# Performance work log

Hardware: AMD Instinct MI355X
Metric: run time of the kernel (lower is better)

Reference implementation:

```python
import jax, jax.numpy as jnp
import numpy as np
from jax import lax

B, TENC, TMEL = 32, 512, 400
E, H, A, P, M, F, K = 512, 512, 512, 256, 128, 32, 31


def setup_inputs() -> dict:
    key = jax.random.key(0)
    ks = jax.random.split(key, 20)
    def rn(i, shape, fan_in):
        return jax.random.normal(ks[i], shape, jnp.float32) / np.float32(np.sqrt(fan_in))
    return dict(
        enc_outputs=jax.random.normal(ks[0], (B, TENC, 2 * E), jnp.float32),
        mel_spec_true=jax.random.normal(ks[1], (B, TMEL, M), jnp.float32),
        text_lens=jax.random.randint(ks[2], (B,), 0, TENC),
        mel_spec_lens=jax.random.randint(ks[3], (B,), 0, TMEL),
        max_text_len=TENC,
        pre_w1=rn(4, (M, P), M), pre_w2=rn(5, (P, P), P),
        attn_wi=rn(6, (P + E, 3 * H), P + E), attn_wh=rn(7, (H, 3 * H), H),
        attn_bi=jnp.zeros((3 * H,), jnp.float32), attn_bh=jnp.zeros((3 * H,), jnp.float32),
        q_w=rn(8, (H, A), H), k_w=rn(9, (2 * E, A), 2 * E),
        score_w=rn(10, (A, 1), A), score_b=jnp.zeros((1,), jnp.float32),
        loc_conv_w=rn(11, (F, 2, K), 2 * K), loc_w=rn(12, (F, A), F), loc_b=jnp.zeros((A,), jnp.float32),
        out_wi=rn(13, (A + H, 3 * H), A + H), out_wh=rn(14, (H, 3 * H), H),
        out_bi=jnp.zeros((3 * H,), jnp.float32), out_bh=jnp.zeros((3 * H,), jnp.float32),
        dec_w=rn(15, (H + A, M), H + A), dec_b=jnp.zeros((M,), jnp.float32),
        gate_w=rn(16, (H + A, 1), H + A), gate_b=jnp.zeros((1,), jnp.float32),
    )


def _gru_step(x, h, wi, wh, bi, bh):
    # single-step torch nn.GRU cell; gate order r, z, n
    gi = x @ wi + bi
    gh = h @ wh + bh
    ir, iz, inn = jnp.split(gi, 3, axis=-1)
    hr, hz, hn = jnp.split(gh, 3, axis=-1)
    r = jax.nn.sigmoid(ir + hr)
    z = jax.nn.sigmoid(iz + hz)
    n = jnp.tanh(inn + r * hn)
    return (1.0 - z) * n + z * h


def reference(enc_outputs, mel_spec_true, text_lens, mel_spec_lens, max_text_len,
              pre_w1, pre_w2, attn_wi, attn_wh, attn_bi, attn_bh,
              q_w, k_w, score_w, score_b, loc_conv_w, loc_w, loc_b,
              out_wi, out_wh, out_bi, out_bh, dec_w, dec_b, gate_w, gate_b):
    Bsz, Tenc, _ = enc_outputs.shape
    Tmel = mel_spec_true.shape[1]
    Hd = attn_wh.shape[0]
    Ad = k_w.shape[1]
    pad = (loc_conv_w.shape[2] - 1) // 2

    keys_p = enc_outputs @ k_w                                # [B,Tenc,A]
    enc_mask = jnp.arange(Tenc)[None, :] > text_lens[:, None]  # True = masked (t > len)

    def prenet(x):  # dropout disabled for determinism
        return jax.nn.relu(jax.nn.relu(x @ pre_w1) @ pre_w2)

    dec_in0 = prenet(jnp.zeros((Bsz, mel_spec_true.shape[2]), enc_outputs.dtype))
    carry0 = (jnp.zeros((Bsz, Hd), jnp.float32), jnp.zeros((Bsz, Hd), jnp.float32),
              jnp.zeros((Bsz, Tenc), jnp.float32), jnp.zeros((Bsz, Tenc), jnp.float32),
              jnp.zeros((Bsz, Ad), jnp.float32), dec_in0)

    def step(carry, _):
        h_attn, h_out, att_w, att_cum, ctx, dec_in = carry
        h_attn = _gru_step(jnp.concatenate([dec_in, ctx], -1), h_attn, attn_wi, attn_wh, attn_bi, attn_bh)
        loc_in = jnp.stack([att_w, att_cum], axis=1)           # [B,2,Tenc]
        loc = lax.conv_general_dilated(loc_in, loc_conv_w, (1,), [(pad, pad)],
                                       dimension_numbers=('NCH', 'OIH', 'NCH'))  # [B,F,Tenc]
        loc = jnp.swapaxes(loc, 1, 2) @ loc_w + loc_b          # [B,Tenc,A]
        q = (h_attn @ q_w)[:, None, :]                         # [B,1,A]
        s = (jnp.tanh(q + keys_p + loc) @ score_w + score_b)[..., 0]  # [B,Tenc]
        s = jnp.where(enc_mask, -jnp.inf, s)
        att_w = jax.nn.softmax(s, axis=1)
        ctx = jnp.einsum('bt,bta->ba', att_w, keys_p)
        att_cum = att_cum + att_w
        h_out = _gru_step(jnp.concatenate([h_attn, ctx], -1), h_out, out_wi, out_wh, out_bi, out_bh)
        att_h = jnp.concatenate([h_out, ctx], -1)
        mel = att_h @ dec_w + dec_b                            # [B,M]
        stop = (att_h @ gate_w + gate_b)[:, 0]                 # [B]
        dec_in = prenet(mel)                                   # teacher_force_ratio = 0
        return (h_attn, h_out, att_w, att_cum, ctx, dec_in), (mel, stop, att_w)

    _, (mels, gates, attns) = lax.scan(step, carry0, None, length=Tmel)
    mels = jnp.swapaxes(mels, 0, 1)    # [B,Tmel,M]
    gates = jnp.swapaxes(gates, 0, 1)  # [B,Tmel]
    attns = jnp.swapaxes(attns, 0, 1)  # [B,Tmel,Tenc]
    mel_mask = jnp.arange(Tmel)[None, :] > mel_spec_lens[:, None]
    masked_mel = jnp.where(mel_mask[:, :, None], 0.0, mels)
    masked_gate = jnp.where(mel_mask, 1000.0, gates)
    return masked_mel, masked_gate, attns, mel_mask
```

## Files before the change

kernel.cpp:

```cpp
#include <hip/hip_runtime.h>
#include <hip/hip_fp16.h>
#include <math.h>

#define NBLK 256
#define NTHR 1024

__device__ __forceinline__ float fast_rcp(float x) {
#if __has_builtin(__builtin_amdgcn_rcpf)
  return __builtin_amdgcn_rcpf(x);
#else
  return 1.f / x;
#endif
}
__device__ __forceinline__ float fast_sigmoid(float x) { return fast_rcp(1.f + __expf(-x)); }
__device__ __forceinline__ float fast_tanh(float x) { return 1.f - 2.f * fast_rcp(1.f + __expf(2.f * x)); }

union HU2 { unsigned int u; __half2 h; };
union HU4 { uint4 u; __half2 h[4]; };
__device__ __forceinline__ float2 cvt2(unsigned int u) { HU2 t; t.u = u; return __half22float2(t.h); }

__device__ __forceinline__ void sta(float* p, float v) {
  __hip_atomic_store(p, v, __ATOMIC_RELAXED, __HIP_MEMORY_SCOPE_AGENT);
}
__device__ __forceinline__ float lda(const float* p) {
  return __hip_atomic_load(p, __ATOMIC_RELAXED, __HIP_MEMORY_SCOPE_AGENT);
}
__device__ __forceinline__ int ldai(const int* p) {
  return __hip_atomic_load(p, __ATOMIC_RELAXED, __HIP_MEMORY_SCOPE_AGENT);
}
__device__ __forceinline__ void ntst(float* p, float v) { __builtin_nontemporal_store(v, p); }

struct Params {
  const float *enc, *pre_w1, *pre_w2, *attn_bi, *attn_bh;
  const float *q_w, *k_w, *score_w, *score_b, *conv_w, *loc_w, *loc_b;
  const float *out_bi, *out_bh, *dec_b, *gate_b;
  const float *attn_wi, *attn_wh, *out_wi, *out_wh, *dec_w, *gate_w;
  const int *text_lens, *mel_lens;
  __half *hkeys, *gw1T, *gw2T, *decT, *pre1T, *pre2T, *gateh, *locwh, *qwT;
  float *hA, *hO, *attw, *attcum, *decin, *ebuf, *zpart, *ctxacc, *ctxacc2, *stateZ;
  float *qbuf;
  int *done, *zdone, *done2, *hAdone, *qdone;
  float *out_mel, *out_gate, *out_attn, *out_mask;
};

__global__ __launch_bounds__(512) void k_keys(Params p) {
  __shared__ float sA[16][132];
  __shared__ float sB[16][68];
  int tid = threadIdx.x;
  int row0 = blockIdx.x * 128, col0 = blockIdx.y * 64;
  float acc[4][4] = {};
  int r = tid >> 2, kq = tid & 3;
  int tx = tid & 15, ty = tid >> 4;
  for (int k0 = 0; k0 < 1024; k0 += 16) {
    __syncthreads();
    float4 a4 = *(const float4*)(p.enc + (size_t)(row0 + r) * 1024 + k0 + kq * 4);
    sA[kq * 4 + 0][r] = a4.x; sA[kq * 4 + 1][r] = a4.y;
    sA[kq * 4 + 2][r] = a4.z; sA[kq * 4 + 3][r] = a4.w;
    if (tid < 256) {
      int kb = tid >> 4, nb = (tid & 15) * 4;
      float4 b4 = *(const float4*)(p.k_w + (size_t)(k0 + kb) * 512 + col0 + nb);
      sB[kb][nb + 0] = b4.x; sB[kb][nb + 1] = b4.y;
      sB[kb][nb + 2] = b4.z; sB[kb][nb + 3] = b4.w;
    }
    __syncthreads();
#pragma unroll
    for (int k = 0; k < 16; k++) {
      float ar[4], br[4];
#pragma unroll
      for (int i = 0; i < 4; i++) { ar[i] = sA[k][ty * 4 + i]; br[i] = sB[k][tx * 4 + i]; }
#pragma unroll
      for (int i = 0; i < 4; i++)
#pragma unroll
        for (int j = 0; j < 4; j++) acc[i][j] = fmaf(ar[i], br[j], acc[i][j]);
    }
  }
#pragma unroll
  for (int i = 0; i < 4; i++)
#pragma unroll
    for (int j = 0; j < 4; j++)
      p.hkeys[(size_t)(row0 + ty * 4 + i) * 512 + col0 + tx * 4 + j] = __float2half(acc[i][j]);
}

__global__ __launch_bounds__(256) void k_repack(Params p) {
  const int gsz = gridDim.x * 256;
  const int t0 = blockIdx.x * 256 + threadIdx.x;
  for (int i = t0; i < 1280 * 512; i += gsz) {
    int r = i >> 9, u = i & 511;
    const float* src = (r < 768) ? p.attn_wi + (size_t)r * 1536 : p.attn_wh + (size_t)(r - 768) * 1536;
    __half2* d = (__half2*)(p.gw1T + ((size_t)i << 2));
    d[0] = __halves2half2(__float2half(src[u]), __float2half(src[512 + u]));
    d[1] = __halves2half2(__float2half(src[1024 + u]), __float2half(0.f));
  }
  for (int i = t0; i < 1536 * 512; i += gsz) {
    int r = i >> 9, u = i & 511;
    const float* src = (r < 1024) ? p.out_wi + (size_t)r * 1536 : p.out_wh + (size_t)(r - 1024) * 1536;
    __half2* d = (__half2*)(p.gw2T + ((size_t)i << 2));
    d[0] = __halves2half2(__float2half(src[u]), __float2half(src[512 + u]));
    d[1] = __halves2half2(__float2half(src[1024 + u]), __float2half(0.f));
  }
  for (int i = t0; i < 512 * 512; i += gsz) {
    int k = i >> 9, a = i & 511;
    p.qwT[(size_t)a * 512 + k] = __float2half(p.q_w[(size_t)k * 512 + a]);
  }
  for (int i = t0; i < 1024 * 128; i += gsz) {
    int k = i >> 7, m = i & 127;
    p.decT[(size_t)m * 1024 + k] = __float2half(p.dec_w[(size_t)k * 128 + m]);
  }
  for (int i = t0; i < 1024; i += gsz) p.gateh[i] = __float2half(p.gate_w[i]);
  for (int i = t0; i < 16384; i += gsz) p.locwh[i] = __float2half(p.loc_w[i]);
  for (int i = t0; i < 128 * 256; i += gsz) {
    int m = i >> 8, pc = i & 255;
    p.pre1T[(size_t)pc * 128 + m] = __float2half(p.pre_w1[(size_t)m * 256 + pc]);
  }
  for (int i = t0; i < 256 * 256; i += gsz) {
    int k = i >> 8, pc = i & 255;
    p.pre2T[(size_t)pc * 256 + k] = __float2half(p.pre_w2[(size_t)k * 256 + pc]);
  }
  for (int i = t0; i < 106496; i += gsz) p.stateZ[i] = 0.f;
  for (int i = t0; i < 16384; i += gsz) p.ctxacc[i] = 0.f;
  for (int i = t0; i < 16384; i += gsz) p.ctxacc2[i] = 0.f;
  for (int i = t0; i < 512; i += gsz) p.qdone[i] = 0;
  for (int i = t0; i < 2048; i += gsz) p.zdone[i] = 0;
  for (int i = t0; i < 12800; i += gsz) {
    int b = i / 400, t = i - b * 400;
    p.out_mask[i] = (t > p.mel_lens[b]) ? 1.f : 0.f;
  }
}

struct SMemMega {
  __half keysL[64 * 512];
  float ctxL[4][520];
  float hA2[4][520];
  float hO2[4][520];
  float invZ[4];
  union {
    struct { float x[4][264]; float4 part4[16][64]; } gr;
    struct { float locS[64][33]; float aw[94]; float ac[94]; float hA_s[512];
             float qS[512]; float qp2[16][64]; float cpred[8][512]; float eS[64]; } s3;
    struct { float xh[1024]; float red[1024]; float mel[128]; float p1[256]; } s6;
  } u;
};

__device__ __forceinline__ void gchunk(const uint2* __restrict__ w,
                                       const float* __restrict__ x, int ks,
                                       int j0, int j1,
                                       float& a0, float& a1, float& a2) {
#pragma unroll 8
  for (int j = j0; j < j1; ++j) {
    uint2 wv = w[(size_t)j << 13];
    float xv = x[ks + (j << 4)];
    float2 f0 = cvt2(wv.x);
    float nf = cvt2(wv.y).x;
    a0 = fmaf(xv, f0.x, a0);
    a1 = fmaf(xv, f0.y, a1);
    a2 = fmaf(xv, nf, a2);
  }
}

__global__ __launch_bounds__(NTHR) void mega(Params p) {
  __shared__ SMemMega sm;
  const int blk = blockIdx.x, tid = threadIdx.x;
  const int ug = blk & 31, bg = blk >> 5, b0 = bg * 4;
  const int bS = blk & 31, t8 = blk >> 5, t0g = t8 << 6;

  const int u_ = tid & 15, b2_ = (tid >> 4) & 3, ks_ = tid >> 6;
  const int uG_ = (ug << 4) + u_;
  const uint2* w1 = (const uint2*)p.gw1T + ((size_t)ks_ << 9) + uG_;
  const uint2* w2 = (const uint2*)p.gw2T + ((size_t)ks_ << 9) + uG_;

  {
    const uint4* src = (const uint4*)(p.hkeys + (((size_t)(bS << 9) + t0g) << 9));
    uint4* dst = (uint4*)sm.keysL;
    for (int i = tid; i < 4096; i += NTHR) dst[i] = src[i];
    for (int i = tid; i < 2048; i += NTHR) sm.ctxL[i >> 9][i & 511] = 0.f;
  }
  __syncthreads();

  float g1r = 0.f, g1z = 0.f, g1ni = 0.f, g1nh = 0.f;

#pragma clang loop unroll(disable)
  for (int step = 0; step < 400; step++) {
    const int par = step & 1;
    float* hA_prev = p.hA + par * 16384;
    float* hA_next = p.hA + (par ^ 1) * 16384;
    float* hO_prev = p.hO + par * 16384;
    float* hO_next = p.hO + (par ^ 1) * 16384;
    float* cCur = par ? p.ctxacc2 : p.ctxacc;
    float* cNxt = par ? p.ctxacc : p.ctxacc2;

    float r2 = 0.f, z2 = 0.f, ni2 = 0.f, nh2 = 0.f;

    {
      if (step > 0) {
        if (tid < 4) {
          while (ldai(&p.done2[(b0 + tid) * 16]) < 4 * step)
            __builtin_amdgcn_s_sleep(2);
        }
        __syncthreads();
      }
      for (int i = tid; i < 1024; i += NTHR)
        sm.u.gr.x[i >> 8][i & 255] = lda(&p.decin[((b0 + (i >> 8)) << 8) + (i & 255)]);
      for (int i = tid; i < 2048; i += NTHR)
        sm.hO2[i >> 9][i & 511] = lda(&hO_prev[((b0 + (i >> 9)) << 9) + (i & 511)]);
      __syncthreads();
      gchunk(w1, &sm.u.gr.x[b2_][0], ks_, 0, 16, g1r, g1z, g1ni);
      sm.u.gr.part4[ks_][(u_ << 2) + b2_] = make_float4(g1r, g1z, g1ni, g1nh);
      __syncthreads();
      if (tid < 64) {
        int uu = tid >> 2, bb2 = tid & 3;
        float4 s = make_float4(0.f, 0.f, 0.f, 0.f);
#pragma unroll
        for (int l = 0; l < 16; l++) {
          float4 v = sm.u.gr.part4[l][(uu << 2) + bb2];
          s.x += v.x; s.y += v.y; s.z += v.z; s.w += v.w;
        }
        int uGf = (ug << 4) + uu;
        float r = fast_sigmoid(s.x + p.attn_bi[uGf] + p.attn_bh[uGf]);
        float z = fast_sigmoid(s.y + p.attn_bi[512 + uGf] + p.attn_bh[512 + uGf]);
        float n = fast_tanh(s.z + p.attn_bi[1024 + uGf] + r * (s.w + p.attn_bh[1024 + uGf]));
        float hv = lda(&hA_prev[((b0 + bb2) << 9) + uGf]);
        sta(&hA_next[((b0 + bb2) << 9) + uGf], (1.f - z) * n + z * hv);
      }
      asm volatile("s_waitcnt vmcnt(0)" ::: "memory");
      if (tid < 4) atomicAdd(&p.hAdone[(b0 + tid) * 16], 1);
      gchunk(w2, &sm.hO2[b2_][0] - 1024, ks_, 64, 96, r2, z2, nh2);
    }

    {
      for (int j = tid; j < 94; j += NTHR) {
        int pp = t0g - 15 + j;
        bool ok = (unsigned)pp < 512u;
        sm.u.s3.aw[j] = ok ? lda(&p.attw[(bS << 9) + pp]) : 0.f;
        sm.u.s3.ac[j] = ok ? lda(&p.attcum[(bS << 9) + pp]) : 0.f;
      }
      if (tid == 0) {
        while (ldai(&p.hAdone[bS * 16]) < 32 * (step + 1))
          __builtin_amdgcn_s_sleep(2);
      }
      __syncthreads();
      if (t8 == 0) {
        for (int i = tid; i < 512; i += NTHR) sta(&cNxt[(bS << 9) + i], 0.f);
      }
      if (tid < 512) sm.u.s3.hA_s[tid] = lda(&hA_next[(bS << 9) + tid]);
      __syncthreads();
      {
        int a = tid & 63, ks = tid >> 6;
        const HU4* qp = (const HU4*)(p.qwT + (size_t)(t0g + a) * 512 + ks * 32);
        float q0 = 0.f, q1 = 0.f;
#pragma unroll
        for (int it = 0; it < 4; it++) {
          HU4 raw = qp[it];
          int kb = ks * 32 + it * 8;
#pragma unroll
          for (int h2 = 0; h2 < 4; h2++) {
            float2 w = __half22float2(raw.h[h2]);
            q0 = fmaf(sm.u.s3.hA_s[kb + h2 * 2], w.x, q0);
            q1 = fmaf(sm.u.s3.hA_s[kb + h2 * 2 + 1], w.y, q1);
          }
        }
        sm.u.s3.qp2[ks][a] = q0 + q1;
      }
      __syncthreads();
      if (tid < 64) {
        float s = 0.f;
#pragma unroll
        for (int l = 0; l < 16; l++) s += sm.u.s3.qp2[l][tid];
        sta(&p.qbuf[(bS << 9) + t0g + tid], s + p.loc_b[t0g + tid]);
      }
      if (tid == 0) {
        asm volatile("s_waitcnt vmcnt(0)" ::: "memory");
        atomicAdd(&p.qdone[bS * 16], 1);
      }
      const int tlen = p.text_lens[bS];
      for (int i = tid; i < 2048; i += NTHR) {
        int tt = i >> 5, f = i & 31;
        const float* w0 = p.conv_w + f * 62;
        float a = 0.f;
#pragma unroll
        for (int k = 0; k < 31; k++)
          a = fmaf(w0[k], sm.u.s3.aw[tt + k], fmaf(w0[31 + k], sm.u.s3.ac[tt + k], a));
        sm.u.s3.locS[tt][f] = a;
      }
      if (tid == 0) {
        while (ldai(&p.qdone[bS * 16]) < 8 * (step + 1))
          __builtin_amdgcn_s_sleep(2);
      }
      __syncthreads();
      if (tid < 512) sm.u.s3.qS[tid] = lda(&p.qbuf[(bS << 9) + tid]);
      __syncthreads();
      const int lane = tid & 63, wv = tid >> 6;
      float acc[4][8];
      float4 qA = *(const float4*)&sm.u.s3.qS[lane * 8];
      float4 qB = *(const float4*)&sm.u.s3.qS[lane * 8 + 4];
#pragma unroll
      for (int j = 0; j < 4; j++) {
        int tL = wv * 4 + j;
        HU4 raw; raw.u = *(const uint4*)&sm.keysL[tL * 512 + lane * 8];
        float2 k0 = __half22float2(raw.h[0]), k1 = __half22float2(raw.h[1]);
        float2 k2 = __half22float2(raw.h[2]), k3 = __half22float2(raw.h[3]);
        acc[j][0] = qA.x + k0.x; acc[j][1] = qA.y + k0.y;
        acc[j][2] = qA.z + k1.x; acc[j][3] = qA.w + k1.y;
        acc[j][4] = qB.x + k2.x; acc[j][5] = qB.y + k2.y;
        acc[j][6] = qB.z + k3.x; acc[j][7] = qB.w + k3.y;
      }
#pragma unroll 4
      for (int f = 0; f < 32; f++) {
        HU4 rw; rw.u = *(const uint4*)(p.locwh + (size_t)f * 512 + lane * 8);
        float2 w0 = __half22float2(rw.h[0]), w1 = __half22float2(rw.h[1]);
        float2 w2v = __half22float2(rw.h[2]), w3 = __half22float2(rw.h[3]);
#pragma unroll
        for (int j = 0; j < 4; j++) {
          float lf = sm.u.s3.locS[wv * 4 + j][f];
          acc[j][0] = fmaf(lf, w0.x, acc[j][0]); acc[j][1] = fmaf(lf, w0.y, acc[j][1]);
          acc[j][2] = fmaf(lf, w1.x, acc[j][2]); acc[j][3] = fmaf(lf, w1.y, acc[j][3]);
          acc[j][4] = fmaf(lf, w2v.x, acc[j][4]); acc[j][5] = fmaf(lf, w2v.y, acc[j][5]);
          acc[j][6] = fmaf(lf, w3.x, acc[j][6]); acc[j][7] = fmaf(lf, w3.y, acc[j][7]);
        }
      }
      float4 sA = *(const float4*)(p.score_w + lane * 8);
      float4 sB = *(const float4*)(p.score_w + lane * 8 + 4);
      float sbias = p.score_b[0];
      float e_reg[4];
#pragma unroll
      for (int j = 0; j < 4; j++) {
        float pv = fast_tanh(acc[j][0]) * sA.x + fast_tanh(acc[j][1]) * sA.y +
                   fast_tanh(acc[j][2]) * sA.z + fast_tanh(acc[j][3]) * sA.w +
                   fast_tanh(acc[j][4]) * sB.x + fast_tanh(acc[j][5]) * sB.y +
                   fast_tanh(acc[j][6]) * sB.z + fast_tanh(acc[j][7]) * sB.w;
#pragma unroll
        for (int off = 32; off > 0; off >>= 1) pv += __shfl_xor(pv, off, 64);
        int t = t0g + wv * 4 + j;
        e_reg[j] = (t > tlen) ? 0.f : __expf(pv + sbias);
      }
      if (lane == 0) {
#pragma unroll
        for (int j = 0; j < 4; j++) sm.u.s3.eS[wv * 4 + j] = e_reg[j];
      }
      float cp[8] = {0.f, 0.f, 0.f, 0.f, 0.f, 0.f, 0.f, 0.f};
#pragma unroll
      for (int j = 0; j < 4; j++) {
        int tL = wv * 4 + j;
        HU4 raw; raw.u = *(const uint4*)&sm.keysL[tL * 512 + lane * 8];
        float2 k0 = __half22float2(raw.h[0]), k1 = __half22float2(raw.h[1]);
        float2 k2 = __half22float2(raw.h[2]), k3 = __half22float2(raw.h[3]);
        float e = e_reg[j];
        cp[0] = fmaf(e, k0.x, cp[0]); cp[1] = fmaf(e, k0.y, cp[1]);
        cp[2] = fmaf(e, k1.x, cp[2]); cp[3] = fmaf(e, k1.y, cp[3]);
        cp[4] = fmaf(e, k2.x, cp[4]); cp[5] = fmaf(e, k2.y, cp[5]);
        cp[6] = fmaf(e, k3.x, cp[6]); cp[7] = fmaf(e, k3.y, cp[7]);
      }
      __syncthreads();
      if (wv < 8) {
        float4* r0 = (float4*)&sm.u.s3.cpred[wv][lane * 8];
        r0[0] = make_float4(cp[0], cp[1], cp[2], cp[3]);
        r0[1] = make_float4(cp[4], cp[5], cp[6], cp[7]);
      }
      __syncthreads();
      if (wv >= 8) {
        float* r0 = &sm.u.s3.cpred[wv - 8][lane * 8];
#pragma unroll
        for (int i = 0; i < 8; i++) r0[i] += cp[i];
      }
      __syncthreads();
      if (tid < 512) {
        float s = 0.f;
#pragma unroll
        for (int j = 0; j < 8; j++) s += sm.u.s3.cpred[j][tid];
        atomicAdd(&cCur[(bS << 9) + tid], s);
      }
      if (tid < 64) {
        float e = sm.u.s3.eS[tid];
        sta(&p.ebuf[(bS << 9) + t0g + tid], e);
        float z = e;
#pragma unroll
        for (int off = 32; off > 0; off >>= 1) z += __shfl_xor(z, off, 64);
        if (tid == 0) sta(&p.zpart[bS * 8 + t8], z);
      }
      if (tid < 512 && (tid & 63) == 0) {
        asm volatile("s_waitcnt vmcnt(0)" ::: "memory");
        atomicAdd(&p.zdone[bS * 16], 1);
      }
      if (tid < 4) {
        while (ldai(&p.hAdone[(b0 + tid) * 16]) < 32 * (step + 1))
          __builtin_amdgcn_s_sleep(2);
      }
      __syncthreads();
      for (int i = tid; i < 2048; i += NTHR)
        sm.hA2[i >> 9][i & 511] = lda(&hA_next[((b0 + (i >> 9)) << 9) + (i & 511)]);
      __syncthreads();
      gchunk(w2, &sm.hA2[b2_][0], ks_, 0, 32, r2, z2, ni2);
    }

    {
      if (tid < 4) {
        while (ldai(&p.zdone[(b0 + tid) * 16]) < 64 * (step + 1))
          __builtin_amdgcn_s_sleep(2);
        float Z = 0.f;
#pragma unroll
        for (int j = 0; j < 8; j++) Z += lda(&p.zpart[(b0 + tid) * 8 + j]);
        sm.invZ[tid] = fast_rcp(Z);
      }
      __syncthreads();
      for (int i = tid; i < 2048; i += NTHR) {
        int b2 = i >> 9, a = i & 511;
        sm.ctxL[b2][a] = lda(&cCur[((b0 + b2) << 9) + a]) * sm.invZ[b2];
      }
      if (ug < 4) {
        const int bb = b0 + ug;
        if (tid < 512) {
          float v = lda(&p.ebuf[(bb << 9) + tid]) * sm.invZ[ug];
          sta(&p.attw[(bb << 9) + tid], v);
          float oc = lda(&p.attcum[(bb << 9) + tid]);
          sta(&p.attcum[(bb << 9) + tid], oc + v);
          ntst(&p.out_attn[(size_t)bb * 204800 + (size_t)step * 512 + tid], v);
        }
      }
      __syncthreads();
      gchunk(w2, &sm.ctxL[b2_][0] - 512, ks_, 32, 64, r2, z2, ni2);
      sm.u.gr.part4[ks_][(u_ << 2) + b2_] = make_float4(r2, z2, ni2, nh2);
      __syncthreads();
      if (tid < 64) {
        int uu = tid >> 2, bb2 = tid & 3;
        float4 s = make_float4(0.f, 0.f, 0.f, 0.f);
#pragma unroll
        for (int l = 0; l < 16; l++) {
          float4 v = sm.u.gr.part4[l][(uu << 2) + bb2];
          s.x += v.x; s.y += v.y; s.z += v.z; s.w += v.w;
        }
        int uGf = (ug << 4) + uu;
        float r = fast_sigmoid(s.x + p.out_bi[uGf] + p.out_bh[uGf]);
        float z = fast_sigmoid(s.y + p.out_bi[512 + uGf] + p.out_bh[512 + uGf]);
        float n = fast_tanh(s.z + p.out_bi[1024 + uGf] + r * (s.w + p.out_bh[1024 + uGf]));
        float hv = sm.hO2[bb2][uGf];
        sta(&hO_next[((b0 + bb2) << 9) + uGf], (1.f - z) * n + z * hv);
      }
      asm volatile("s_waitcnt vmcnt(0)" ::: "memory");
      if (tid < 4) atomicAdd(&p.done[(b0 + tid) * 16], 1);
      if (ug < 4) {
        const int bb = b0 + ug;
        if (tid == 0) {
          int target = 32 * (step + 1);
          while (ldai(&p.done[bb * 16]) < target)
            __builtin_amdgcn_s_sleep(2);
        }
        __syncthreads();
        sm.u.s6.xh[tid] = (tid < 512) ? lda(&hO_next[(bb << 9) + tid])
                                      : sm.ctxL[ug][tid - 512];
        __syncthreads();
        bool masked = step > p.mel_lens[bb];
        {
          int m = tid & 127, ks = tid >> 7;
          const HU4* dp = (const HU4*)(p.decT + (size_t)m * 1024 + ks * 128);
          float a = 0.f;
#pragma unroll 4
          for (int it = 0; it < 16; it++) {
            HU4 raw = dp[it];
            int kb = ks * 128 + it * 8;
#pragma unroll
            for (int h2 = 0; h2 < 4; h2++) {
              float2 w = __half22float2(raw.h[h2]);
              a = fmaf(sm.u.s6.xh[kb + h2 * 2], w.x, a);
              a = fmaf(sm.u.s6.xh[kb + h2 * 2 + 1], w.y, a);
            }
          }
          sm.u.s6.red[tid] = a;
        }
        __syncthreads();
        if (tid < 128) {
          float mv = p.dec_b[tid];
#pragma unroll
          for (int j = 0; j < 8; j++) mv += sm.u.s6.red[tid + j * 128];
          sm.u.s6.mel[tid] = mv;
          ntst(&p.out_mel[(size_t)bb * 51200 + (size_t)step * 128 + tid], masked ? 0.f : mv);
        }
        __syncthreads();
        sm.u.s6.red[tid] = sm.u.s6.xh[tid] * __half2float(p.gateh[tid]);
        __syncthreads();
        if (tid < 64) {
          float g = 0.f;
#pragma unroll
          for (int j = 0; j < 16; j++) g += sm.u.s6.red[tid + j * 64];
#pragma unroll
          for (int off = 32; off > 0; off >>= 1) g += __shfl_xor(g, off, 64);
          if (tid == 0) ntst(&p.out_gate[bb * 400 + step], masked ? 1000.f : (g + p.gate_b[0]));
        }
        __syncthreads();
        {
          int pc = tid & 255, ks = tid >> 8;
          const HU4* wp = (const HU4*)(p.pre1T + (size_t)pc * 128 + ks * 32);
          float a = 0.f;
#pragma unroll
          for (int it = 0; it < 4; it++) {
            HU4 raw = wp[it];
            int kb = ks * 32 + it * 8;
#pragma unroll
            for (int h2 = 0; h2 < 4; h2++) {
              float2 w = __half22float2(raw.h[h2]);
              a = fmaf(sm.u.s6.mel[kb + h2 * 2], w.x, a);
              a = fmaf(sm.u.s6.mel[kb + h2 * 2 + 1], w.y, a);
            }
          }
          sm.u.s6.red[tid] = a;
        }
        __syncthreads();
        if (tid < 256) {
          float a = sm.u.s6.red[tid] + sm.u.s6.red[tid + 256] +
                    sm.u.s6.red[tid + 512] + sm.u.s6.red[tid + 768];
          sm.u.s6.p1[tid] = fmaxf(a, 0.f);
        }
        __syncthreads();
        {
          int pc = tid & 255, ks = tid >> 8;
          const HU4* wp = (const HU4*)(p.pre2T + (size_t)pc * 256 + ks * 64);
          float a = 0.f;
#pragma unroll
          for (int it = 0; it < 8; it++) {
            HU4 raw = wp[it];
            int kb = ks * 64 + it * 8;
#pragma unroll
            for (int h2 = 0; h2 < 4; h2++) {
              float2 w = __half22float2(raw.h[h2]);
              a = fmaf(sm.u.s6.p1[kb + h2 * 2], w.x, a);
              a = fmaf(sm.u.s6.p1[kb + h2 * 2 + 1], w.y, a);
            }
          }
          sm.u.s6.red[tid] = a;
        }
        __syncthreads();
        if (tid < 256) {
          float a = sm.u.s6.red[tid] + sm.u.s6.red[tid + 256] +
                    sm.u.s6.red[tid + 512] + sm.u.s6.red[tid + 768];
          sta(&p.decin[(bb << 8) + tid], fmaxf(a, 0.f));
        }
        if (tid < 256 && (tid & 63) == 0) {
          asm volatile("s_waitcnt vmcnt(0)" ::: "memory");
          atomicAdd(&p.done2[bb * 16], 1);
        }
      }
      g1r = 0.f; g1z = 0.f; g1ni = 0.f; g1nh = 0.f;
      if (step < 399) {
        gchunk(w1, &sm.ctxL[b2_][0] - 256, ks_, 16, 48, g1r, g1z, g1ni);
        gchunk(w1, &sm.hA2[b2_][0] - 768, ks_, 48, 80, g1r, g1z, g1nh);
      }
    }
  }
}

extern "C" void kernel_launch(void* const* d_in, const int* in_sizes, int n_in,
                              void* d_out, int out_size, void* d_ws, size_t ws_size,
                              hipStream_t stream) {
  Params p;
  p.enc       = (const float*)d_in[0];
  p.text_lens = (const int*)d_in[2];
  p.mel_lens  = (const int*)d_in[3];
  p.pre_w1    = (const float*)d_in[5];
  p.pre_w2    = (const float*)d_in[6];
  p.attn_wi   = (const float*)d_in[7];
  p.attn_wh   = (const float*)d_in[8];
  p.attn_bi   = (const float*)d_in[9];
  p.attn_bh   = (const float*)d_in[10];
  p.q_w       = (const float*)d_in[11];
  p.k_w       = (const float*)d_in[12];
  p.score_w   = (const float*)d_in[13];
  p.score_b   = (const float*)d_in[14];
  p.conv_w    = (const float*)d_in[15];
  p.loc_w     = (const float*)d_in[16];
  p.loc_b     = (const float*)d_in[17];
  p.out_wi    = (const float*)d_in[18];
  p.out_wh    = (const float*)d_in[19];
  p.out_bi    = (const float*)d_in[20];
  p.out_bh    = (const float*)d_in[21];
  p.dec_w     = (const float*)d_in[22];
  p.dec_b     = (const float*)d_in[23];
  p.gate_w    = (const float*)d_in[24];
  p.gate_b    = (const float*)d_in[25];

  float* ws = (float*)d_ws;
  p.hkeys  = (__half*)(ws);
  p.gw1T   = (__half*)(ws + 4194304);
  p.gw2T   = (__half*)(ws + 5505024);
  p.decT   = (__half*)(ws + 7077888);
  p.pre1T  = (__half*)(ws + 7143424);
  p.pre2T  = (__half*)(ws + 7159808);
  p.gateh  = (__half*)(ws + 7192576);
  p.locwh  = (__half*)(ws + 7193088);
  p.qwT    = (__half*)(ws + 7201280);
  p.hA     = ws + 7332352;
  p.hO     = ws + 7365120;
  p.attw   = ws + 7397888;
  p.attcum = ws + 7414272;
  p.decin  = ws + 7430656;
  p.stateZ = p.hA;
  p.ebuf   = ws + 7438848;
  p.zpart  = ws + 7455232;
  p.ctxacc = ws + 7455488;
  p.qdone  = (int*)(ws + 7471904);
  p.ctxacc2 = ws + 7472416;
  p.zdone  = (int*)(ws + 7488800);
  p.done2  = (int*)(ws + 7489312);
  p.hAdone = (int*)(ws + 7489824);
  p.done   = (int*)(ws + 7490336);
  p.qbuf   = ws + 7490848;
  float* out = (float*)d_out;
  p.out_mel  = out;
  p.out_gate = out + 1638400;
  p.out_attn = out + 1651200;
  p.out_mask = out + 8204800;

  k_repack<<<2048, 256, 0, stream>>>(p);
  k_keys<<<dim3(128, 8), 512, 0, stream>>>(p);
  void* args[] = { (void*)&p };
  hipLaunchCooperativeKernel((const void*)mega, dim3(NBLK), dim3(NTHR), args, 0, stream);
}
```

Before: 37.60 ms.

## Fuse query projection into GRU blocks and compute decoder/prenet redundantly per block

The query projection moves into the attention-GRU update: each block multiplies its 16-unit hidden slice by q_w and atomically accumulates partial queries into double-buffered global accumulators. This removes the separate qbuf/qdone phase and one grid-wide wait. The mel/gate/prenet stage is now computed redundantly by every block for its 4 batch rows, with hidden state, hO and decin kept in shared memory. That removes the done2 handshake and the global decin reload, at the cost of more weight reads and atomics per step.

```diff
diff --git a/kernel.cpp b/kernel.cpp
--- a/kernel.cpp
+++ b/kernel.cpp
@@ -38,8 +38,8 @@
   const int *text_lens, *mel_lens;
   __half *hkeys, *gw1T, *gw2T, *decT, *pre1T, *pre2T, *gateh, *locwh, *qwT;
   float *hA, *hO, *attw, *attcum, *decin, *ebuf, *zpart, *ctxacc, *ctxacc2, *stateZ;
-  float *qbuf;
-  int *done, *zdone, *done2, *hAdone, *qdone;
+  float *qacc1, *qacc2;
+  int *done, *zdone, *done2, *hAdone;
   float *out_mel, *out_gate, *out_attn, *out_mask;
 };
 
@@ -98,10 +98,6 @@
     d[0] = __halves2half2(__float2half(src[u]), __float2half(src[512 + u]));
     d[1] = __halves2half2(__float2half(src[1024 + u]), __float2half(0.f));
   }
-  for (int i = t0; i < 512 * 512; i += gsz) {
-    int k = i >> 9, a = i & 511;
-    p.qwT[(size_t)a * 512 + k] = __float2half(p.q_w[(size_t)k * 512 + a]);
-  }
   for (int i = t0; i < 1024 * 128; i += gsz) {
     int k = i >> 7, m = i & 127;
     p.decT[(size_t)m * 1024 + k] = __float2half(p.dec_w[(size_t)k * 128 + m]);
@@ -119,7 +115,8 @@
   for (int i = t0; i < 106496; i += gsz) p.stateZ[i] = 0.f;
   for (int i = t0; i < 16384; i += gsz) p.ctxacc[i] = 0.f;
   for (int i = t0; i < 16384; i += gsz) p.ctxacc2[i] = 0.f;
-  for (int i = t0; i < 512; i += gsz) p.qdone[i] = 0;
+  for (int i = t0; i < 16384; i += gsz) p.qacc1[i] = 0.f;
+  for (int i = t0; i < 16384; i += gsz) p.qacc2[i] = 0.f;
   for (int i = t0; i < 2048; i += gsz) p.zdone[i] = 0;
   for (int i = t0; i < 12800; i += gsz) {
     int b = i / 400, t = i - b * 400;
@@ -131,13 +128,14 @@
   __half keysL[64 * 512];
   float ctxL[4][520];
   float hA2[4][520];
-  float hO2[4][520];
+  float hOL[4][520];
+  float decinL[4][264];
   float invZ[4];
   union {
-    struct { float x[4][264]; float4 part4[16][64]; } gr;
-    struct { float locS[64][33]; float aw[94]; float ac[94]; float hA_s[512];
-             float qS[512]; float qp2[16][64]; float cpred[8][512]; float eS[64]; } s3;
-    struct { float xh[1024]; float red[1024]; float mel[128]; float p1[256]; } s6;
+    struct { float4 part4[16][64]; float hAslice[4][16]; } gr;
+    struct { float locS[64][33]; float aw[94]; float ac[94];
+             float qS[512]; float cpred[8][512]; float eS[64]; } s3;
+    struct { float xh[4][1032]; float red[4][264]; float mel[4][132]; float p1[4][264]; } s6;
   } u;
 };
 
@@ -172,7 +170,12 @@
     const uint4* src = (const uint4*)(p.hkeys + (((size_t)(bS << 9) + t0g) << 9));
     uint4* dst = (uint4*)sm.keysL;
     for (int i = tid; i < 4096; i += NTHR) dst[i] = src[i];
-    for (int i = tid; i < 2048; i += NTHR) sm.ctxL[i >> 9][i & 511] = 0.f;
+    for (int i = tid; i < 2048; i += NTHR) {
+      sm.ctxL[i >> 9][i & 511] = 0.f;
+      sm.hA2[i >> 9][i & 511] = 0.f;
+      sm.hOL[i >> 9][i & 511] = 0.f;
+    }
+    for (int i = tid; i < 1024; i += NTHR) sm.decinL[i >> 8][i & 255] = 0.f;
   }
   __syncthreads();
 
@@ -181,29 +184,17 @@
 #pragma clang loop unroll(disable)
   for (int step = 0; step < 400; step++) {
     const int par = step & 1;
-    float* hA_prev = p.hA + par * 16384;
     float* hA_next = p.hA + (par ^ 1) * 16384;
-    float* hO_prev = p.hO + par * 16384;
     float* hO_next = p.hO + (par ^ 1) * 16384;
     float* cCur = par ? p.ctxacc2 : p.ctxacc;
     float* cNxt = par ? p.ctxacc : p.ctxacc2;
+    float* qCur = par ? p.qacc2 : p.qacc1;
+    float* qNxt = par ? p.qacc1 : p.qacc2;
 
     float r2 = 0.f, z2 = 0.f, ni2 = 0.f, nh2 = 0.f;
 
     {
-      if (step > 0) {
-        if (tid < 4) {
-          while (ldai(&p.done2[(b0 + tid) * 16]) < 4 * step)
-            __builtin_amdgcn_s_sleep(2);
-        }
-        __syncthreads();
-      }
-      for (int i = tid; i < 1024; i += NTHR)
-        sm.u.gr.x[i >> 8][i & 255] = lda(&p.decin[((b0 + (i >> 8)) << 8) + (i & 255)]);
-      for (int i = tid; i < 2048; i += NTHR)
-        sm.hO2[i >> 9][i & 511] = lda(&hO_prev[((b0 + (i >> 9)) << 9) + (i & 511)]);
-      __syncthreads();
-      gchunk(w1, &sm.u.gr.x[b2_][0], ks_, 0, 16, g1r, g1z, g1ni);
+      gchunk(w1, &sm.decinL[b2_][0], ks_, 0, 16, g1r, g1z, g1ni);
       sm.u.gr.part4[ks_][(u_ << 2) + b2_] = make_float4(g1r, g1z, g1ni, g1nh);
       __syncthreads();
       if (tid < 64) {
@@ -218,59 +209,55 @@
         float r = fast_sigmoid(s.x + p.attn_bi[uGf] + p.attn_bh[uGf]);
         float z = fast_sigmoid(s.y + p.attn_bi[512 + uGf] + p.attn_bh[512 + uGf]);
         float n = fast_tanh(s.z + p.attn_bi[1024 + uGf] + r * (s.w + p.attn_bh[1024 + uGf]));
-        float hv = lda(&hA_prev[((b0 + bb2) << 9) + uGf]);
-        sta(&hA_next[((b0 + bb2) << 9) + uGf], (1.f - z) * n + z * hv);
-      }
-      asm volatile("s_waitcnt vmcnt(0)" ::: "memory");
-      if (tid < 4) atomicAdd(&p.hAdone[(b0 + tid) * 16], 1);
-      gchunk(w2, &sm.hO2[b2_][0] - 1024, ks_, 64, 96, r2, z2, nh2);
+        float hv = sm.hA2[bb2][uGf];
+        float hnew = (1.f - z) * n + z * hv;
+        sta(&hA_next[((b0 + bb2) << 9) + uGf], hnew);
+        sm.u.gr.hAslice[bb2][uu] = hnew;
+      }
+      __syncthreads();
+      {
+        int a = tid & 511, bh = tid >> 9;
+        const float* qw = p.q_w + ((size_t)(ug << 4)) * 512 + a;
+        float s0 = 0.f, s1 = 0.f;
+#pragma unroll
+        for (int u = 0; u < 16; u++) {
+          float w = qw[(size_t)u * 512];
+          s0 = fmaf(sm.u.gr.hAslice[bh * 2][u], w, s0);
+          s1 = fmaf(sm.u.gr.hAslice[bh * 2 + 1][u], w, s1);
+        }
+        atomicAdd(&qCur[((b0 + bh * 2) << 9) + a], s0);
+        atomicAdd(&qCur[((b0 + bh * 2 + 1) << 9) + a], s1);
+      }
+      if ((tid & 63) == 0) {
+        asm volatile("s_waitcnt vmcnt(0)" ::: "memory");
+        atomicAdd(&p.hAdone[(b0 + ((tid >> 6) & 3)) * 16], 0);
+      }
+      if ((tid & 63) == 0) {
+        atomicAdd(&p.hAdone[(b0 + ((tid >> 6) & 3)) * 16], 1);
+      }
+      gchunk(w2, &sm.hOL[b2_][0] - 1024, ks_, 64, 96, r2, z2, nh2);
     }
 
     {
+      if (tid == 0) {
+        while (ldai(&p.hAdone[bS * 16]) < 128 * (step + 1))
+          __builtin_amdgcn_s_sleep(2);
+      }
+      __syncthreads();
       for (int j = tid; j < 94; j += NTHR) {
         int pp = t0g - 15 + j;
         bool ok = (unsigned)pp < 512u;
         sm.u.s3.aw[j] = ok ? lda(&p.attw[(bS << 9) + pp]) : 0.f;
         sm.u.s3.ac[j] = ok ? lda(&p.attcum[(bS << 9) + pp]) : 0.f;
       }
-      if (tid == 0) {
-        while (ldai(&p.hAdone[bS * 16]) < 32 * (step + 1))
-          __builtin_amdgcn_s_sleep(2);
-      }
-      __syncthreads();
       if (t8 == 0) {
-        for (int i = tid; i < 512; i += NTHR) sta(&cNxt[(bS << 9) + i], 0.f);
-      }
-      if (tid < 512) sm.u.s3.hA_s[tid] = lda(&hA_next[(bS << 9) + tid]);
-      __syncthreads();
-      {
-        int a = tid & 63, ks = tid >> 6;
-        const HU4* qp = (const HU4*)(p.qwT + (size_t)(t0g + a) * 512 + ks * 32);
-        float q0 = 0.f, q1 = 0.f;
-#pragma unroll
-        for (int it = 0; it < 4; it++) {
-          HU4 raw = qp[it];
-          int kb = ks * 32 + it * 8;
-#pragma unroll
-          for (int h2 = 0; h2 < 4; h2++) {
-            float2 w = __half22float2(raw.h[h2]);
-            q0 = fmaf(sm.u.s3.hA_s[kb + h2 * 2], w.x, q0);
-            q1 = fmaf(sm.u.s3.hA_s[kb + h2 * 2 + 1], w.y, q1);
-          }
-        }
-        sm.u.s3.qp2[ks][a] = q0 + q1;
-      }
-      __syncthreads();
-      if (tid < 64) {
-        float s = 0.f;
-#pragma unroll
-        for (int l = 0; l < 16; l++) s += sm.u.s3.qp2[l][tid];
-        sta(&p.qbuf[(bS << 9) + t0g + tid], s + p.loc_b[t0g + tid]);
-      }
-      if (tid == 0) {
-        asm volatile("s_waitcnt vmcnt(0)" ::: "memory");
-        atomicAdd(&p.qdone[bS * 16], 1);
-      }
+        for (int i = tid; i < 512; i += NTHR) {
+          sta(&cNxt[(bS << 9) + i], 0.f);
+          sta(&qNxt[(bS << 9) + i], 0.f);
+        }
+      }
+      if (tid < 512) sm.u.s3.qS[tid] = lda(&qCur[(bS << 9) + tid]) + p.loc_b[tid];
+      __syncthreads();
       const int tlen = p.text_lens[bS];
       for (int i = tid; i < 2048; i += NTHR) {
         int tt = i >> 5, f = i & 31;
@@ -281,12 +268,6 @@
           a = fmaf(w0[k], sm.u.s3.aw[tt + k], fmaf(w0[31 + k], sm.u.s3.ac[tt + k], a));
         sm.u.s3.locS[tt][f] = a;
       }
-      if (tid == 0) {
-        while (ldai(&p.qdone[bS * 16]) < 8 * (step + 1))
-          __builtin_amdgcn_s_sleep(2);
-      }
-      __syncthreads();
-      if (tid < 512) sm.u.s3.qS[tid] = lda(&p.qbuf[(bS << 9) + tid]);
       __syncthreads();
       const int lane = tid & 63, wv = tid >> 6;
       float acc[4][8];
@@ -381,7 +362,7 @@
         atomicAdd(&p.zdone[bS * 16], 1);
       }
       if (tid < 4) {
-        while (ldai(&p.hAdone[(b0 + tid) * 16]) < 32 * (step + 1))
+        while (ldai(&p.hAdone[(b0 + tid) * 16]) < 128 * (step + 1))
           __builtin_amdgcn_s_sleep(2);
       }
       __syncthreads();
@@ -405,15 +386,13 @@
         int b2 = i >> 9, a = i & 511;
         sm.ctxL[b2][a] = lda(&cCur[((b0 + b2) << 9) + a]) * sm.invZ[b2];
       }
-      if (ug < 4) {
+      if (ug < 4 && tid < 512) {
         const int bb = b0 + ug;
-        if (tid < 512) {
-          float v = lda(&p.ebuf[(bb << 9) + tid]) * sm.invZ[ug];
-          sta(&p.attw[(bb << 9) + tid], v);
-          float oc = lda(&p.attcum[(bb << 9) + tid]);
-          sta(&p.attcum[(bb << 9) + tid], oc + v);
-          ntst(&p.out_attn[(size_t)bb * 204800 + (size_t)step * 512 + tid], v);
-        }
+        float v = lda(&p.ebuf[(bb << 9) + tid]) * sm.invZ[ug];
+        sta(&p.attw[(bb << 9) + tid], v);
+        float oc = lda(&p.attcum[(bb << 9) + tid]);
+        sta(&p.attcum[(bb << 9) + tid], oc + v);
+        ntst(&p.out_attn[(size_t)bb * 204800 + (size_t)step * 512 + tid], v);
       }
       __syncthreads();
       gchunk(w2, &sm.ctxL[b2_][0] - 512, ks_, 32, 64, r2, z2, ni2);
@@ -431,117 +410,118 @@
         float r = fast_sigmoid(s.x + p.out_bi[uGf] + p.out_bh[uGf]);
         float z = fast_sigmoid(s.y + p.out_bi[512 + uGf] + p.out_bh[512 + uGf]);
         float n = fast_tanh(s.z + p.out_bi[1024 + uGf] + r * (s.w + p.out_bh[1024 + uGf]));
-        float hv = sm.hO2[bb2][uGf];
+        float hv = sm.hOL[bb2][uGf];
         sta(&hO_next[((b0 + bb2) << 9) + uGf], (1.f - z) * n + z * hv);
       }
       asm volatile("s_waitcnt vmcnt(0)" ::: "memory");
       if (tid < 4) atomicAdd(&p.done[(b0 + tid) * 16], 1);
-      if (ug < 4) {
-        const int bb = b0 + ug;
-        if (tid == 0) {
-          int target = 32 * (step + 1);
-          while (ldai(&p.done[bb * 16]) < target)
-            __builtin_amdgcn_s_sleep(2);
-        }
-        __syncthreads();
-        sm.u.s6.xh[tid] = (tid < 512) ? lda(&hO_next[(bb << 9) + tid])
-                                      : sm.ctxL[ug][tid - 512];
-        __syncthreads();
-        bool masked = step > p.mel_lens[bb];
-        {
-          int m = tid & 127, ks = tid >> 7;
-          const HU4* dp = (const HU4*)(p.decT + (size_t)m * 1024 + ks * 128);
-          float a = 0.f;
-#pragma unroll 4
-          for (int it = 0; it < 16; it++) {
-            HU4 raw = dp[it];
-            int kb = ks * 128 + it * 8;
-#pragma unroll
-            for (int h2 = 0; h2 < 4; h2++) {
-              float2 w = __half22float2(raw.h[h2]);
-              a = fmaf(sm.u.s6.xh[kb + h2 * 2], w.x, a);
-              a = fmaf(sm.u.s6.xh[kb + h2 * 2 + 1], w.y, a);
-            }
-          }
-          sm.u.s6.red[tid] = a;
-        }
-        __syncthreads();
-        if (tid < 128) {
-          float mv = p.dec_b[tid];
-#pragma unroll
-          for (int j = 0; j < 8; j++) mv += sm.u.s6.red[tid + j * 128];
-          sm.u.s6.mel[tid] = mv;
-          ntst(&p.out_mel[(size_t)bb * 51200 + (size_t)step * 128 + tid], masked ? 0.f : mv);
-        }
-        __syncthreads();
-        sm.u.s6.red[tid] = sm.u.s6.xh[tid] * __half2float(p.gateh[tid]);
-        __syncthreads();
-        if (tid < 64) {
-          float g = 0.f;
-#pragma unroll
-          for (int j = 0; j < 16; j++) g += sm.u.s6.red[tid + j * 64];
-#pragma unroll
-          for (int off = 32; off > 0; off >>= 1) g += __shfl_xor(g, off, 64);
-          if (tid == 0) ntst(&p.out_gate[bb * 400 + step], masked ? 1000.f : (g + p.gate_b[0]));
-        }
-        __syncthreads();
-        {
-          int pc = tid & 255, ks = tid >> 8;
-          const HU4* wp = (const HU4*)(p.pre1T + (size_t)pc * 128 + ks * 32);
-          float a = 0.f;
-#pragma unroll
-          for (int it = 0; it < 4; it++) {
-            HU4 raw = wp[it];
-            int kb = ks * 32 + it * 8;
-#pragma unroll
-            for (int h2 = 0; h2 < 4; h2++) {
-              float2 w = __half22float2(raw.h[h2]);
-              a = fmaf(sm.u.s6.mel[kb + h2 * 2], w.x, a);
-              a = fmaf(sm.u.s6.mel[kb + h2 * 2 + 1], w.y, a);
-            }
-          }
-          sm.u.s6.red[tid] = a;
-        }
-        __syncthreads();
-        if (tid < 256) {
-          float a = sm.u.s6.red[tid] + sm.u.s6.red[tid + 256] +
-                    sm.u.s6.red[tid + 512] + sm.u.s6.red[tid + 768];
-          sm.u.s6.p1[tid] = fmaxf(a, 0.f);
-        }
-        __syncthreads();
-        {
-          int pc = tid & 255, ks = tid >> 8;
-          const HU4* wp = (const HU4*)(p.pre2T + (size_t)pc * 256 + ks * 64);
-          float a = 0.f;
-#pragma unroll
-          for (int it = 0; it < 8; it++) {
-            HU4 raw = wp[it];
-            int kb = ks * 64 + it * 8;
-#pragma unroll
-            for (int h2 = 0; h2 < 4; h2++) {
-              float2 w = __half22float2(raw.h[h2]);
-              a = fmaf(sm.u.s6.p1[kb + h2 * 2], w.x, a);
-              a = fmaf(sm.u.s6.p1[kb + h2 * 2 + 1], w.y, a);
-            }
-          }
-          sm.u.s6.red[tid] = a;
-        }
-        __syncthreads();
-        if (tid < 256) {
-          float a = sm.u.s6.red[tid] + sm.u.s6.red[tid + 256] +
-                    sm.u.s6.red[tid + 512] + sm.u.s6.red[tid + 768];
-          sta(&p.decin[(bb << 8) + tid], fmaxf(a, 0.f));
-        }
-        if (tid < 256 && (tid & 63) == 0) {
-          asm volatile("s_waitcnt vmcnt(0)" ::: "memory");
-          atomicAdd(&p.done2[bb * 16], 1);
-        }
-      }
       g1r = 0.f; g1z = 0.f; g1ni = 0.f; g1nh = 0.f;
       if (step < 399) {
         gchunk(w1, &sm.ctxL[b2_][0] - 256, ks_, 16, 48, g1r, g1z, g1ni);
         gchunk(w1, &sm.hA2[b2_][0] - 768, ks_, 48, 80, g1r, g1z, g1nh);
       }
+      if (tid < 4) {
+        while (ldai(&p.done[(b0 + tid) * 16]) < 32 * (step + 1))
+          __builtin_amdgcn_s_sleep(2);
+      }
+      __syncthreads();
+      for (int i = tid; i < 4096; i += NTHR) {
+        int b = i >> 10, j = i & 1023;
+        float v;
+        if (j < 512) { v = lda(&hO_next[((b0 + b) << 9) + j]); sm.hOL[b][j] = v; }
+        else v = sm.ctxL[b][j - 512];
+        sm.u.s6.xh[b][j] = v;
+      }
+      __syncthreads();
+      {
+        int b = tid >> 8, t = tid & 255, m = t & 127, kh = t >> 7;
+        const HU4* dp = (const HU4*)(p.decT + (size_t)m * 1024 + kh * 512);
+        const float* xb = &sm.u.s6.xh[b][kh * 512];
+        float a = 0.f;
+#pragma unroll 8
+        for (int it = 0; it < 64; it++) {
+          HU4 raw = dp[it];
+          int kb = it * 8;
+#pragma unroll
+          for (int h2 = 0; h2 < 4; h2++) {
+            float2 w = __half22float2(raw.h[h2]);
+            a = fmaf(xb[kb + h2 * 2], w.x, a);
+            a = fmaf(xb[kb + h2 * 2 + 1], w.y, a);
+          }
+        }
+        sm.u.s6.red[b][t] = a;
+      }
+      __syncthreads();
+      if (tid < 512) {
+        int b = tid >> 7, m = tid & 127;
+        float mv = p.dec_b[m] + sm.u.s6.red[b][m] + sm.u.s6.red[b][m + 128];
+        sm.u.s6.mel[b][m] = mv;
+        if (ug < 4 && b == ug) {
+          int bb = b0 + b;
+          bool masked = step > p.mel_lens[bb];
+          ntst(&p.out_mel[(size_t)bb * 51200 + (size_t)step * 128 + m], masked ? 0.f : mv);
+        }
+      }
+      __syncthreads();
+      {
+        int b = tid >> 8, t = tid & 255;
+        float g = 0.f;
+#pragma unroll
+        for (int j = 0; j < 4; j++)
+          g += sm.u.s6.xh[b][t + j * 256] * __half2float(p.gateh[t + j * 256]);
+        sm.u.s6.red[b][t] = g;
+      }
+      __syncthreads();
+      if (ug < 4 && tid < 256) {
+        int b = tid >> 6, l = tid & 63;
+        if (b == ug) {
+          float g = sm.u.s6.red[b][l] + sm.u.s6.red[b][l + 64] +
+                    sm.u.s6.red[b][l + 128] + sm.u.s6.red[b][l + 192];
+#pragma unroll
+          for (int off = 32; off > 0; off >>= 1) g += __shfl_xor(g, off, 64);
+          if (l == 0) {
+            int bb = b0 + b;
+            bool masked = step > p.mel_lens[bb];
+            ntst(&p.out_gate[bb * 400 + step], masked ? 1000.f : (g + p.gate_b[0]));
+          }
+        }
+      }
+      {
+        int b = tid >> 8, pc = tid & 255;
+        const HU4* wp = (const HU4*)(p.pre1T + (size_t)pc * 128);
+        float a = 0.f;
+#pragma unroll
+        for (int it = 0; it < 16; it++) {
+          HU4 raw = wp[it];
+          int kb = it * 8;
+#pragma unroll
+          for (int h2 = 0; h2 < 4; h2++) {
+            float2 w = __half22float2(raw.h[h2]);
+            a = fmaf(sm.u.s6.mel[b][kb + h2 * 2], w.x, a);
+            a = fmaf(sm.u.s6.mel[b][kb + h2 * 2 + 1], w.y, a);
+          }
+        }
+        sm.u.s6.p1[b][pc] = fmaxf(a, 0.f);
+      }
+      __syncthreads();
+      {
+        int b = tid >> 8, pc = tid & 255;
+        const HU4* wp = (const HU4*)(p.pre2T + (size_t)pc * 256);
+        float a = 0.f;
+#pragma unroll 8
+        for (int it = 0; it < 32; it++) {
+          HU4 raw = wp[it];
+          int kb = it * 8;
+#pragma unroll
+          for (int h2 = 0; h2 < 4; h2++) {
+            float2 w = __half22float2(raw.h[h2]);
+            a = fmaf(sm.u.s6.p1[b][kb + h2 * 2], w.x, a);
+            a = fmaf(sm.u.s6.p1[b][kb + h2 * 2 + 1], w.y, a);
+          }
+        }
+        sm.decinL[b][pc] = fmaxf(a, 0.f);
+      }
+      __syncthreads();
     }
   }
 }
@@ -594,13 +574,13 @@
   p.ebuf   = ws + 7438848;
   p.zpart  = ws + 7455232;
   p.ctxacc = ws + 7455488;
-  p.qdone  = (int*)(ws + 7471904);
   p.ctxacc2 = ws + 7472416;
   p.zdone  = (int*)(ws + 7488800);
   p.done2  = (int*)(ws + 7489312);
   p.hAdone = (int*)(ws + 7489824);
   p.done   = (int*)(ws + 7490336);
-  p.qbuf   = ws + 7490848;
+  p.qacc1  = ws + 7490848;
+  p.qacc2  = ws + 7507232;
   float* out = (float*)d_out;
   p.out_mel  = out;
   p.out_gate = out + 1638400;
```

Result: slower. 58.25 ms (+54.9%).
